# Performance work log

Hardware: AMD Instinct MI355X
Metric: run time of the kernel (lower is better)

Reference implementation:

```python
import jax, jax.numpy as jnp
import numpy as np

N = 50000        # node_num
E = 1600000      # num edges
F_IN = 8
HID = 1000
R = 100          # robustness_length


def setup_inputs() -> dict:
    key = jax.random.key(0)
    ks = jax.random.split(key, 16)
    X = jax.random.normal(ks[0], (N, F_IN), dtype=jnp.float32)
    edge_index = jax.random.randint(ks[1], (2, E), 0, N, dtype=jnp.int64)
    s = 1.0 / np.sqrt(F_IN)
    # SAGEConv mean-aggr params (PyG: out = lin_l(aggr) + lin_r(x), lin_r has no bias)
    lin_l_w = jax.random.uniform(ks[2], (1, F_IN), jnp.float32, -s, s)
    lin_l_b = jax.random.uniform(ks[3], (1,), jnp.float32, -s, s)
    lin_r_w = jax.random.uniform(ks[4], (1, F_IN), jnp.float32, -s, s)
    # SAGEConv max-aggr params
    lin_l1_w = jax.random.uniform(ks[5], (1, F_IN), jnp.float32, -s, s)
    lin_l1_b = jax.random.uniform(ks[6], (1,), jnp.float32, -s, s)
    lin_r1_w = jax.random.uniform(ks[7], (1, F_IN), jnp.float32, -s, s)
    # MLP params
    s0 = 1.0 / np.sqrt(N)
    W0 = jax.random.uniform(ks[8], (HID, N), jnp.float32, -s0, s0)
    b0 = jax.random.uniform(ks[9], (HID,), jnp.float32, -s0, s0)
    s1 = 1.0 / np.sqrt(HID)
    W1 = jax.random.uniform(ks[10], (HID, HID), jnp.float32, -s1, s1)
    b1 = jax.random.uniform(ks[11], (HID,), jnp.float32, -s1, s1)
    W2 = jax.random.uniform(ks[12], (R, HID), jnp.float32, -s1, s1)
    b2 = jax.random.uniform(ks[13], (R,), jnp.float32, -s1, s1)
    return dict(X=X, edge_index=edge_index,
                lin_l_w=lin_l_w, lin_l_b=lin_l_b, lin_r_w=lin_r_w,
                lin_l1_w=lin_l1_w, lin_l1_b=lin_l1_b, lin_r1_w=lin_r1_w,
                W0=W0, b0=b0, W1=W1, b1=b1, W2=W2, b2=b2)


def reference(X, edge_index, lin_l_w, lin_l_b, lin_r_w,
              lin_l1_w, lin_l1_b, lin_r1_w,
              W0, b0, W1, b1, W2, b2):
    src, dst = edge_index[0], edge_index[1]
    msgs = X[src]  # [E, F_IN] gathered neighbor features
    cnt = jax.ops.segment_sum(jnp.ones((E,), jnp.float32), dst, num_segments=N)
    # mean aggregation (empty -> 0)
    agg_mean = jax.ops.segment_sum(msgs, dst, num_segments=N) / jnp.maximum(cnt, 1.0)[:, None]
    # max aggregation (empty -> 0, per PyG scatter-max fill)
    agg_max = jax.ops.segment_max(msgs, dst, num_segments=N)
    agg_max = jnp.where(cnt[:, None] > 0, agg_max, 0.0)
    # SAGEConv: lin_l(aggr) + lin_r(x)
    h_mean = jax.nn.relu(agg_mean @ lin_l_w.T + lin_l_b + X @ lin_r_w.T)   # [N,1]
    h_max = jax.nn.relu(agg_max @ lin_l1_w.T + lin_l1_b + X @ lin_r1_w.T)  # [N,1]
    x = (h_mean + h_max).reshape(-1)  # [N]
    X_embedding = x
    h = jax.nn.relu(W0 @ x + b0)
    h = jax.nn.relu(W1 @ h + b1)
    out = jax.nn.relu(W2 @ h + b2)
    return (X_embedding, out)
```

## Files before the change

kernel.cpp:

```cpp
#include <hip/hip_runtime.h>

#define N_NODES 50000
#define N_EDGES 1600000
#define F_IN 8
#define HID 1000
#define R_OUT 100

#define BSHIFT 7
#define NPB 128
#define NB 391
#define CAP_B 4608
#define CHUNK 4096
#define NBIN_BLOCKS ((N_EDGES + CHUNK - 1) / CHUNK)
#define NCHUNK0 25


__device__ __forceinline__ unsigned fkey(float f) {
    unsigned b = __float_as_uint(f);
    return (b & 0x80000000u) ? ~b : (b | 0x80000000u);
}
__device__ __forceinline__ float funkey(unsigned k) {
    unsigned b = (k & 0x80000000u) ? (k & 0x7fffffffu) : ~k;
    return __uint_as_float(b);
}

__global__ void init_kernel(unsigned* __restrict__ p, int nzero,
                            const float* __restrict__ b0, float* __restrict__ h0) {
    int i = blockIdx.x * blockDim.x + threadIdx.x;
    if (i < nzero) p[i] = 0u;
    if (i < HID) h0[i] = b0[i];
}

__global__ void bin_kernel(const int* __restrict__ ei,
                           const float* __restrict__ X,
                           const float* __restrict__ wl,
                           int* __restrict__ cursor,
                           unsigned* __restrict__ binned,
                           int* __restrict__ ovf_cnt,
                           float* __restrict__ ovf_sum,
                           unsigned* __restrict__ ovf_max) {
    __shared__ unsigned sEntry[CHUNK];
    __shared__ unsigned short sBucket[CHUNK];
    __shared__ int hist[NB];
    __shared__ int pos[NB];
    __shared__ int base[NB];
    int tid = threadIdx.x;
    int e0 = blockIdx.x * CHUNK;
    int e1 = e0 + CHUNK;
    if (e1 > N_EDGES) e1 = N_EDGES;
    int ne = e1 - e0;

    for (int i = tid; i < NB; i += 256) { hist[i] = 0; pos[i] = 0; }
    __syncthreads();

    for (int j = tid; j < ne; j += 256) {
        int src = ei[e0 + j];
        int dst = ei[N_EDGES + e0 + j];
        int b = dst >> BSHIFT;
        sEntry[j] = (unsigned)src | ((unsigned)(dst & (NPB - 1)) << 16);
        sBucket[j] = (unsigned short)b;
        atomicAdd(&hist[b], 1);
    }
    __syncthreads();

    for (int b = tid; b < NB; b += 256) {
        int h = hist[b];
        base[b] = (h > 0) ? atomicAdd(&cursor[b], h) : 0;
    }
    __syncthreads();

    for (int j = tid; j < ne; j += 256) {
        unsigned entry = sEntry[j];
        int b = sBucket[j];
        int p = atomicAdd(&pos[b], 1);
        int gp = base[b] + p;
        if (gp < CAP_B) {
            binned[(size_t)b * CAP_B + gp] = entry;
        } else {
            int src = entry & 0xFFFF;
            int dst = b * NPB + (int)(entry >> 16);
            const float4* X4 = (const float4*)(X + src * F_IN);
            float4 a = X4[0], bb = X4[1];
            float f[8] = {a.x, a.y, a.z, a.w, bb.x, bb.y, bb.z, bb.w};
            float d = 0.f;
#pragma unroll
            for (int k = 0; k < 8; ++k) d += f[k] * wl[k];
            atomicAdd(&ovf_cnt[dst], 1);
            atomicAdd(&ovf_sum[dst], d);
            unsigned* mb = ovf_max + (size_t)dst * 8;
#pragma unroll
            for (int k = 0; k < 8; ++k) atomicMax(&mb[k], fkey(f[k]));
        }
    }
}

__global__ void agg_kernel(const int* __restrict__ cursor,
                           const unsigned* __restrict__ binned,
                           const int* __restrict__ ovf_cnt,
                           const float* __restrict__ ovf_sum,
                           const unsigned* __restrict__ ovf_max,
                           const float* __restrict__ X,
                           const float* __restrict__ lin_l_w,
                           const float* __restrict__ lin_l_b,
                           const float* __restrict__ lin_r_w,
                           const float* __restrict__ lin_l1_w,
                           const float* __restrict__ lin_l1_b,
                           const float* __restrict__ lin_r1_w,
                           float* __restrict__ xemb) {
    __shared__ unsigned sEntry[CAP_B];
    __shared__ unsigned sSorted[CAP_B];
    __shared__ int sCnt[NPB];
    __shared__ int sOff[NPB];
    __shared__ int sPos[NPB];

    int b = blockIdx.x;
    int tid = threadIdx.x;
    int n = cursor[b];
    if (n > CAP_B) n = CAP_B;

    if (tid < NPB) { sCnt[tid] = 0; sPos[tid] = 0; }
    __syncthreads();

    for (int j = tid; j < n; j += 512) {
        unsigned e = binned[(size_t)b * CAP_B + j];
        sEntry[j] = e;
        atomicAdd(&sCnt[e >> 16], 1);
    }
    __syncthreads();

    if (tid == 0) {
        int run = 0;
#pragma unroll
        for (int i = 0; i < NPB; ++i) { sOff[i] = run; run += sCnt[i]; }
    }
    __syncthreads();

    for (int j = tid; j < n; j += 512) {
        unsigned e = sEntry[j];
        int d = e >> 16;
        int p = atomicAdd(&sPos[d], 1);
        sSorted[sOff[d] + p] = e;
    }
    __syncthreads();

    int nl = tid >> 2;
    int r = tid & 3;
    int beg = sOff[nl];
    int cnt = sCnt[nl];

    float wl[8];
#pragma unroll
    for (int k = 0; k < 8; ++k) wl[k] = lin_l_w[k];

    float sumdot = 0.f;
    float mx[8];
#pragma unroll
    for (int k = 0; k < 8; ++k) mx[k] = -INFINITY;

    for (int j = beg + r; j < beg + cnt; j += 4) {
        int src = sSorted[j] & 0xFFFF;
        const float4* X4 = (const float4*)(X + src * F_IN);
        float4 a = X4[0], bb = X4[1];
        float f[8] = {a.x, a.y, a.z, a.w, bb.x, bb.y, bb.z, bb.w};
        float d = 0.f;
#pragma unroll
        for (int k = 0; k < 8; ++k) d += f[k] * wl[k];
        sumdot += d;
#pragma unroll
        for (int k = 0; k < 8; ++k) mx[k] = fmaxf(mx[k], f[k]);
    }
#pragma unroll
    for (int m = 1; m <= 2; m <<= 1) {
        sumdot += __shfl_xor(sumdot, m, 4);
#pragma unroll
        for (int k = 0; k < 8; ++k) mx[k] = fmaxf(mx[k], __shfl_xor(mx[k], m, 4));
    }

    if (r == 0) {
        int node = b * NPB + nl;
        if (node < N_NODES) {
            int oc = ovf_cnt[node];
            int total = cnt + oc;
            float sd = sumdot + ovf_sum[node];
            if (oc > 0) {
                const unsigned* mb = ovf_max + (size_t)node * 8;
#pragma unroll
                for (int k = 0; k < 8; ++k) mx[k] = fmaxf(mx[k], funkey(mb[k]));
            }
            float c = (float)total;
            float mean_dot = sd / fmaxf(c, 1.0f);
            const float4* X4 = (const float4*)(X + node * F_IN);
            float4 a = X4[0], bb = X4[1];
            float f[8] = {a.x, a.y, a.z, a.w, bb.x, bb.y, bb.z, bb.w};
            float dr = 0.f, dr1 = 0.f, dmax = 0.f;
            bool nonempty = (total > 0);
#pragma unroll
            for (int k = 0; k < 8; ++k) {
                float m = nonempty ? mx[k] : 0.0f;
                dmax += m * lin_l1_w[k];
                dr   += f[k] * lin_r_w[k];
                dr1  += f[k] * lin_r1_w[k];
            }
            float hm = fmaxf(mean_dot + lin_l_b[0] + dr, 0.f);
            float hx = fmaxf(dmax + lin_l1_b[0] + dr1, 0.f);
            xemb[node] = hm + hx;
        }
    }
}


template <int BLOCK, int NCHUNK>
__global__ void gemv_accum(const float* __restrict__ W,
                           const float* __restrict__ x,
                           float* __restrict__ y, int cols) {
    int c = blockIdx.x;
    int row = blockIdx.y;
    int chunk = cols / NCHUNK;
    const float4* W4 = (const float4*)(W + (size_t)row * cols + (size_t)c * chunk);
    const float4* x4 = (const float4*)(x + c * chunk);
    int n4 = chunk >> 2;
    float s = 0.f;
    for (int j = threadIdx.x; j < n4; j += BLOCK) {
        float4 w = W4[j], xx = x4[j];
        s += w.x * xx.x + w.y * xx.y + w.z * xx.z + w.w * xx.w;
    }
#pragma unroll
    for (int off = 32; off > 0; off >>= 1) s += __shfl_down(s, off, 64);
    __shared__ float red[BLOCK / 64];
    int t = threadIdx.x;
    if ((t & 63) == 0) red[t >> 6] = s;
    __syncthreads();
    if (t == 0) {
        float tot = 0.f;
#pragma unroll
        for (int w = 0; w < BLOCK / 64; ++w) tot += red[w];
        atomicAdd(&y[row], tot);
    }
}

template <int BLOCK, bool RELUX>
__global__ void gemv_relu(const float* __restrict__ W,
                          const float* __restrict__ x,
                          const float* __restrict__ bias,
                          float* __restrict__ y, int cols) {
    int row = blockIdx.x;
    const float4* W4 = (const float4*)(W + (size_t)row * cols);
    const float4* x4 = (const float4*)x;
    int n4 = cols >> 2;
    float s = 0.f;
    for (int j = threadIdx.x; j < n4; j += BLOCK) {
        float4 w = W4[j], xx = x4[j];
        if (RELUX) {
            xx.x = fmaxf(xx.x, 0.f); xx.y = fmaxf(xx.y, 0.f);
            xx.z = fmaxf(xx.z, 0.f); xx.w = fmaxf(xx.w, 0.f);
        }
        s += w.x * xx.x + w.y * xx.y + w.z * xx.z + w.w * xx.w;
    }
#pragma unroll
    for (int off = 32; off > 0; off >>= 1) s += __shfl_down(s, off, 64);
    __shared__ float red[BLOCK / 64];
    int t = threadIdx.x;
    if ((t & 63) == 0) red[t >> 6] = s;
    __syncthreads();
    if (t == 0) {
        float tot = 0.f;
#pragma unroll
        for (int w = 0; w < BLOCK / 64; ++w) tot += red[w];
        y[row] = fmaxf(tot + bias[row], 0.f);
    }
}


__global__ void init_ws_fb(unsigned* __restrict__ p, int n) {
    int i = blockIdx.x * blockDim.x + threadIdx.x;
    if (i < n) p[i] = 0u;
}

__global__ void edge_kernel_fb(const int* __restrict__ ei,
                               const float* __restrict__ X,
                               const float* __restrict__ wl,
                               float* __restrict__ sumw,
                               float* __restrict__ cnt,
                               unsigned* __restrict__ maxb) {
    int e = blockIdx.x * blockDim.x + threadIdx.x;
    if (e >= N_EDGES) return;
    int src = ei[e];
    int dst = ei[N_EDGES + e];
    const float4* X4 = (const float4*)(X + src * F_IN);
    float4 a = X4[0], b = X4[1];
    float f[8] = {a.x, a.y, a.z, a.w, b.x, b.y, b.z, b.w};
    float d = 0.f;
#pragma unroll
    for (int k = 0; k < 8; ++k) d += f[k] * wl[k];
    atomicAdd(&sumw[dst], d);
    atomicAdd(&cnt[dst], 1.0f);
    unsigned* mb = maxb + (size_t)dst * 8;
#pragma unroll
    for (int k = 0; k < 8; ++k) atomicMax(&mb[k], fkey(f[k]));
}

__global__ void node_kernel_fb(const float* __restrict__ X,
                               const float* __restrict__ sumw,
                               const float* __restrict__ cnt,
                               const unsigned* __restrict__ maxb,
                               const float* __restrict__ lin_l_b,
                               const float* __restrict__ lin_r_w,
                               const float* __restrict__ lin_l1_w,
                               const float* __restrict__ lin_l1_b,
                               const float* __restrict__ lin_r1_w,
                               float* __restrict__ xout) {
    int i = blockIdx.x * blockDim.x + threadIdx.x;
    if (i >= N_NODES) return;
    float c = cnt[i];
    float mean_dot = sumw[i] / fmaxf(c, 1.0f);
    const float4* X4 = (const float4*)(X + i * F_IN);
    float4 a = X4[0], b = X4[1];
    float f[8] = {a.x, a.y, a.z, a.w, b.x, b.y, b.z, b.w};
    const uint4* M4 = (const uint4*)(maxb + (size_t)i * 8);
    uint4 m0 = M4[0], m1 = M4[1];
    unsigned mk[8] = {m0.x, m0.y, m0.z, m0.w, m1.x, m1.y, m1.z, m1.w};
    float dr = 0.f, dr1 = 0.f, dmax = 0.f;
    bool nonempty = (c > 0.f);
#pragma unroll
    for (int k = 0; k < 8; ++k) {
        float mxv = nonempty ? funkey(mk[k]) : 0.0f;
        dmax += mxv * lin_l1_w[k];
        dr   += f[k] * lin_r_w[k];
        dr1  += f[k] * lin_r1_w[k];
    }
    float hm = fmaxf(mean_dot + lin_l_b[0] + dr, 0.f);
    float hx = fmaxf(dmax + lin_l1_b[0] + dr1, 0.f);
    xout[i] = hm + hx;
}


extern "C" void kernel_launch(void* const* d_in, const int* in_sizes, int n_in,
                              void* d_out, int out_size, void* d_ws, size_t ws_size,
                              hipStream_t stream) {
    const float* X        = (const float*)d_in[0];
    const int*   ei       = (const int*)d_in[1];
    const float* lin_l_w  = (const float*)d_in[2];
    const float* lin_l_b  = (const float*)d_in[3];
    const float* lin_r_w  = (const float*)d_in[4];
    const float* lin_l1_w = (const float*)d_in[5];
    const float* lin_l1_b = (const float*)d_in[6];
    const float* lin_r1_w = (const float*)d_in[7];
    const float* W0       = (const float*)d_in[8];
    const float* b0       = (const float*)d_in[9];
    const float* W1       = (const float*)d_in[10];
    const float* b1       = (const float*)d_in[11];
    const float* W2       = (const float*)d_in[12];
    const float* b2       = (const float*)d_in[13];

    float* xemb = (float*)d_out;
    float* out2 = xemb + N_NODES;

    const size_t zero_words = (size_t)NB + (size_t)N_NODES * 10;
    const size_t need_words = zero_words + (size_t)NB * CAP_B + 2 * HID;
    if (ws_size >= need_words * 4) {
        int*      cursor  = (int*)d_ws;
        int*      ovf_cnt = cursor + NB;
        float*    ovf_sum = (float*)(ovf_cnt + N_NODES);
        unsigned* ovf_max = (unsigned*)(ovf_sum + N_NODES);
        unsigned* binned  = ovf_max + (size_t)N_NODES * 8;
        float*    h0      = (float*)(binned + (size_t)NB * CAP_B);
        float*    h1      = h0 + HID;

        hipLaunchKernelGGL(init_kernel, dim3(((int)zero_words + 255) / 256), dim3(256), 0, stream,
                           (unsigned*)d_ws, (int)zero_words, b0, h0);
        hipLaunchKernelGGL(bin_kernel, dim3(NBIN_BLOCKS), dim3(256), 0, stream,
                           ei, X, lin_l_w, cursor, binned, ovf_cnt, ovf_sum, ovf_max);
        hipLaunchKernelGGL(agg_kernel, dim3(NB), dim3(512), 0, stream,
                           cursor, binned, ovf_cnt, ovf_sum, ovf_max, X,
                           lin_l_w, lin_l_b, lin_r_w, lin_l1_w, lin_l1_b, lin_r1_w, xemb);

        hipLaunchKernelGGL((gemv_accum<256, NCHUNK0>), dim3(NCHUNK0, HID), dim3(256), 0, stream,
                           W0, xemb, h0, N_NODES);
        hipLaunchKernelGGL((gemv_relu<256, true>), dim3(HID), dim3(256), 0, stream,
                           W1, h0, b1, h1, HID);
        hipLaunchKernelGGL((gemv_relu<256, false>), dim3(R_OUT), dim3(256), 0, stream,
                           W2, h1, b2, out2, HID);
    } else {
        float*    sumw = (float*)d_ws;
        float*    cntf = sumw + N_NODES;
        unsigned* maxb = (unsigned*)(cntf + N_NODES);
        float*    h0   = (float*)(maxb + (size_t)N_NODES * 8);
        float*    h1   = h0 + HID;

        int zw = N_NODES * 10;
        hipLaunchKernelGGL(init_ws_fb, dim3((zw + 255) / 256), dim3(256), 0, stream,
                           (unsigned*)d_ws, zw);
        hipLaunchKernelGGL(edge_kernel_fb, dim3((N_EDGES + 255) / 256), dim3(256), 0, stream,
                           ei, X, lin_l_w, sumw, cntf, maxb);
        hipLaunchKernelGGL(node_kernel_fb, dim3((N_NODES + 255) / 256), dim3(256), 0, stream,
                           X, sumw, cntf, maxb, lin_l_b, lin_r_w, lin_l1_w, lin_l1_b,
                           lin_r1_w, xemb);
        hipLaunchKernelGGL((gemv_relu<256, false>), dim3(HID), dim3(256), 0, stream,
                           W0, xemb, b0, h0, N_NODES);
        hipLaunchKernelGGL((gemv_relu<256, false>), dim3(HID), dim3(256), 0, stream,
                           W1, h0, b1, h1, HID);
        hipLaunchKernelGGL((gemv_relu<256, false>), dim3(R_OUT), dim3(256), 0, stream,
                           W2, h1, b2, out2, HID);
    }
}
```

Before: 357.1 us.

## Replace per-bucket LDS sort with shared-memory atomic aggregation and smaller buckets

The aggregation kernel no longer counting-sorts each bucket's edges in shared memory. Each thread now processes edges directly and accumulates sum, count and order-preserving max keys into per-node LDS slots with atomics. Buckets shrink from 128 to 64 nodes, doubling block count and halving per-bucket capacity. The bin kernel reads edge indices as int4 vectors. This removes several barriers and sort passes, but adds LDS atomic contention (8 atomicMax per edge) and may push more edges into the global-atomic overflow path at the smaller capacity.

```diff
diff --git a/kernel.cpp b/kernel.cpp
--- a/kernel.cpp
+++ b/kernel.cpp
@@ -6,10 +6,10 @@
 #define HID 1000
 #define R_OUT 100
 
-#define BSHIFT 7
-#define NPB 128
-#define NB 391
-#define CAP_B 4608
+#define BSHIFT 6
+#define NPB 64
+#define NB 782
+#define CAP_B 2432
 #define CHUNK 4096
 #define NBIN_BLOCKS ((N_EDGES + CHUNK - 1) / CHUNK)
 #define NCHUNK0 25
@@ -53,13 +53,22 @@
     for (int i = tid; i < NB; i += 256) { hist[i] = 0; pos[i] = 0; }
     __syncthreads();
 
-    for (int j = tid; j < ne; j += 256) {
-        int src = ei[e0 + j];
-        int dst = ei[N_EDGES + e0 + j];
-        int b = dst >> BSHIFT;
-        sEntry[j] = (unsigned)src | ((unsigned)(dst & (NPB - 1)) << 16);
-        sBucket[j] = (unsigned short)b;
-        atomicAdd(&hist[b], 1);
+    const int4* s4 = (const int4*)(ei + e0);
+    const int4* d4 = (const int4*)(ei + N_EDGES + e0);
+    int n4 = ne >> 2;
+    for (int j4 = tid; j4 < n4; j4 += 256) {
+        int4 s = s4[j4];
+        int4 d = d4[j4];
+        int jj = j4 << 2;
+        int sv[4] = {s.x, s.y, s.z, s.w};
+        int dv[4] = {d.x, d.y, d.z, d.w};
+#pragma unroll
+        for (int m = 0; m < 4; ++m) {
+            int b = dv[m] >> BSHIFT;
+            sEntry[jj + m] = (unsigned)sv[m] | ((unsigned)(dv[m] & (NPB - 1)) << 16);
+            sBucket[jj + m] = (unsigned short)b;
+            atomicAdd(&hist[b], 1);
+        }
     }
     __syncthreads();
 
@@ -82,11 +91,11 @@
             const float4* X4 = (const float4*)(X + src * F_IN);
             float4 a = X4[0], bb = X4[1];
             float f[8] = {a.x, a.y, a.z, a.w, bb.x, bb.y, bb.z, bb.w};
-            float d = 0.f;
-#pragma unroll
-            for (int k = 0; k < 8; ++k) d += f[k] * wl[k];
+            float dacc = 0.f;
+#pragma unroll
+            for (int k = 0; k < 8; ++k) dacc += f[k] * wl[k];
             atomicAdd(&ovf_cnt[dst], 1);
-            atomicAdd(&ovf_sum[dst], d);
+            atomicAdd(&ovf_sum[dst], dacc);
             unsigned* mb = ovf_max + (size_t)dst * 8;
 #pragma unroll
             for (int k = 0; k < 8; ++k) atomicMax(&mb[k], fkey(f[k]));
@@ -107,85 +116,54 @@
                            const float* __restrict__ lin_l1_b,
                            const float* __restrict__ lin_r1_w,
                            float* __restrict__ xemb) {
-    __shared__ unsigned sEntry[CAP_B];
-    __shared__ unsigned sSorted[CAP_B];
-    __shared__ int sCnt[NPB];
-    __shared__ int sOff[NPB];
-    __shared__ int sPos[NPB];
+    __shared__ float sSum[NPB];
+    __shared__ int   sCnt[NPB];
+    __shared__ unsigned sMax[8][NPB];
 
     int b = blockIdx.x;
     int tid = threadIdx.x;
     int n = cursor[b];
     if (n > CAP_B) n = CAP_B;
 
-    if (tid < NPB) { sCnt[tid] = 0; sPos[tid] = 0; }
-    __syncthreads();
-
-    for (int j = tid; j < n; j += 512) {
-        unsigned e = binned[(size_t)b * CAP_B + j];
-        sEntry[j] = e;
-        atomicAdd(&sCnt[e >> 16], 1);
-    }
-    __syncthreads();
-
-    if (tid == 0) {
-        int run = 0;
-#pragma unroll
-        for (int i = 0; i < NPB; ++i) { sOff[i] = run; run += sCnt[i]; }
-    }
-    __syncthreads();
-
-    for (int j = tid; j < n; j += 512) {
-        unsigned e = sEntry[j];
+    if (tid < NPB) { sSum[tid] = 0.f; sCnt[tid] = 0; }
+    for (int i = tid; i < 8 * NPB; i += 256) ((unsigned*)sMax)[i] = 0u;
+    __syncthreads();
+
+    float wl[8];
+#pragma unroll
+    for (int k = 0; k < 8; ++k) wl[k] = lin_l_w[k];
+
+    const unsigned* blist = binned + (size_t)b * CAP_B;
+    for (int j = tid; j < n; j += 256) {
+        unsigned e = blist[j];
+        int src = e & 0xFFFF;
         int d = e >> 16;
-        int p = atomicAdd(&sPos[d], 1);
-        sSorted[sOff[d] + p] = e;
-    }
-    __syncthreads();
-
-    int nl = tid >> 2;
-    int r = tid & 3;
-    int beg = sOff[nl];
-    int cnt = sCnt[nl];
-
-    float wl[8];
-#pragma unroll
-    for (int k = 0; k < 8; ++k) wl[k] = lin_l_w[k];
-
-    float sumdot = 0.f;
-    float mx[8];
-#pragma unroll
-    for (int k = 0; k < 8; ++k) mx[k] = -INFINITY;
-
-    for (int j = beg + r; j < beg + cnt; j += 4) {
-        int src = sSorted[j] & 0xFFFF;
         const float4* X4 = (const float4*)(X + src * F_IN);
-        float4 a = X4[0], bb = X4[1];
-        float f[8] = {a.x, a.y, a.z, a.w, bb.x, bb.y, bb.z, bb.w};
-        float d = 0.f;
-#pragma unroll
-        for (int k = 0; k < 8; ++k) d += f[k] * wl[k];
-        sumdot += d;
-#pragma unroll
-        for (int k = 0; k < 8; ++k) mx[k] = fmaxf(mx[k], f[k]);
-    }
-#pragma unroll
-    for (int m = 1; m <= 2; m <<= 1) {
-        sumdot += __shfl_xor(sumdot, m, 4);
-#pragma unroll
-        for (int k = 0; k < 8; ++k) mx[k] = fmaxf(mx[k], __shfl_xor(mx[k], m, 4));
-    }
-
-    if (r == 0) {
-        int node = b * NPB + nl;
+        float4 a = X4[0], c = X4[1];
+        float f[8] = {a.x, a.y, a.z, a.w, c.x, c.y, c.z, c.w};
+        float dot = 0.f;
+#pragma unroll
+        for (int k = 0; k < 8; ++k) dot += f[k] * wl[k];
+        atomicAdd(&sSum[d], dot);
+        atomicAdd(&sCnt[d], 1);
+#pragma unroll
+        for (int k = 0; k < 8; ++k) atomicMax(&sMax[k][d], fkey(f[k]));
+    }
+    __syncthreads();
+
+    if (tid < NPB) {
+        int node = b * NPB + tid;
         if (node < N_NODES) {
             int oc = ovf_cnt[node];
-            int total = cnt + oc;
-            float sd = sumdot + ovf_sum[node];
+            int total = sCnt[tid] + oc;
+            float sd = sSum[tid] + ovf_sum[node];
+            unsigned km[8];
+#pragma unroll
+            for (int k = 0; k < 8; ++k) km[k] = sMax[k][tid];
             if (oc > 0) {
                 const unsigned* mb = ovf_max + (size_t)node * 8;
 #pragma unroll
-                for (int k = 0; k < 8; ++k) mx[k] = fmaxf(mx[k], funkey(mb[k]));
+                for (int k = 0; k < 8; ++k) km[k] = (km[k] > mb[k]) ? km[k] : mb[k];
             }
             float c = (float)total;
             float mean_dot = sd / fmaxf(c, 1.0f);
@@ -196,7 +174,7 @@
             bool nonempty = (total > 0);
 #pragma unroll
             for (int k = 0; k < 8; ++k) {
-                float m = nonempty ? mx[k] : 0.0f;
+                float m = nonempty ? funkey(km[k]) : 0.0f;
                 dmax += m * lin_l1_w[k];
                 dr   += f[k] * lin_r_w[k];
                 dr1  += f[k] * lin_r1_w[k];
@@ -370,7 +348,7 @@
                            (unsigned*)d_ws, (int)zero_words, b0, h0);
         hipLaunchKernelGGL(bin_kernel, dim3(NBIN_BLOCKS), dim3(256), 0, stream,
                            ei, X, lin_l_w, cursor, binned, ovf_cnt, ovf_sum, ovf_max);
-        hipLaunchKernelGGL(agg_kernel, dim3(NB), dim3(512), 0, stream,
+        hipLaunchKernelGGL(agg_kernel, dim3(NB), dim3(256), 0, stream,
                            cursor, binned, ovf_cnt, ovf_sum, ovf_max, X,
                            lin_l_w, lin_l_b, lin_r_w, lin_l1_w, lin_l1_b, lin_r1_w, xemb);
 
```

Measured after the change: 357.1 us (median of 2 runs). Within noise of the previous version (-0.0%).
